# Kernel tuning notes

Measured on AMD Instinct MI355X. Metric: run time of the kernel, lower is better.

The kernel has to match this reference:

```python
import jax, jax.numpy as jnp
import numpy as np


def setup_inputs() -> dict:
    key = jax.random.key(0)
    ks = jax.random.split(key, 8)
    B, T, V, D, H, C = 1024, 80, 50000, 300, 300, 3
    sent = jax.random.randint(ks[0], (B, T), 0, V, dtype=jnp.int32)
    lens = jax.random.randint(ks[1], (B,), 1, T + 1, dtype=jnp.int32)
    emb = jax.random.normal(ks[2], (V, D), dtype=jnp.float32) * 0.1
    Wx = jax.random.normal(ks[3], (D, 4 * H), dtype=jnp.float32) * 0.05
    Wh = jax.random.normal(ks[4], (H, 4 * H), dtype=jnp.float32) * 0.05
    b = jnp.zeros((4 * H,), dtype=jnp.float32)
    Wout = jax.random.normal(ks[5], (H, C), dtype=jnp.float32) * 0.05
    bout = jnp.zeros((C,), dtype=jnp.float32)
    return {"sent": sent, "lens": lens, "emb": emb, "Wx": Wx, "Wh": Wh,
            "b": b, "Wout": Wout, "bout": bout}


def _lstm_masked(x, mask, Wx, Wh, b, H):
    # x: [B, T, D], mask: [B, T] float. Scan over time keeping h,c in carry.
    B = x.shape[0]
    h0 = jnp.zeros((B, H), dtype=x.dtype)
    c0 = jnp.zeros((B, H), dtype=x.dtype)

    def step(carry, inp):
        h, c = carry
        xt, mt = inp                      # xt: [B, D], mt: [B]
        gates = xt @ Wx + h @ Wh + b      # [B, 4H]
        i, f, g, o = jnp.split(gates, 4, axis=-1)
        i, f, o = jax.nn.sigmoid(i), jax.nn.sigmoid(f), jax.nn.sigmoid(o)
        g = jnp.tanh(g)
        c_new = f * c + i * g
        h_new = o * jnp.tanh(c_new)
        m = mt[:, None]
        h = m * h_new + (1.0 - m) * h     # mask-based state blending
        c = m * c_new + (1.0 - m) * c
        return (h, c), None

    xs = (jnp.swapaxes(x, 0, 1), jnp.swapaxes(mask, 0, 1))  # time-major
    (h, c), _ = jax.lax.scan(step, (h0, c0), xs)
    return h


def reference(sent, lens, emb, Wx, Wh, b, Wout, bout):
    T = sent.shape[1]
    H = Wh.shape[0]
    x = emb[sent]                                         # [B, T, D]
    mask = (jnp.arange(T)[None, :] < lens[:, None]).astype(x.dtype)  # [B, T]
    h = _lstm_masked(x, mask, Wx, Wh, b, H)
    logit = h @ Wout + bout                               # [B, C]
    return logit
```

## Files before the change

### kernel.cpp

```cpp
#include <hip/hip_runtime.h>
#include <hip/hip_fp16.h>


typedef float    f32x4 __attribute__((ext_vector_type(4)));
typedef _Float16 f16;
typedef _Float16 f16x8 __attribute__((ext_vector_type(8)));
typedef unsigned long long u64;
typedef unsigned int       u32;

#define NB    1024
#define TT    80
#define NV    50000
#define ND    300
#define KP    320
#define NKT   10
#define SL    75
#define SLP   80
#define NTPG  5
#define NTIL  20
#define TPB   256
#define GRID  256
#define NSLAB 8

#define TAGMASK 0x0001000100010001ULL

#define OFF_EMB   0
#define OFF_WHP   32000000
#define OFF_WXP   32819200
#define OFF_HBUF  33638400
#define HBUF_SZ   (NB * KP)
#define OFF_HF32  38881280
#define WS_NEED   40110080

__global__ __launch_bounds__(256) void absa_prep_emb(
    const float* __restrict__ emb, f16* __restrict__ embb) {
  int i = blockIdx.x * 256 + threadIdx.x;
  if (i >= NV * KP / 8) return;
  int flat = i * 8;
  int row  = flat / KP;
  int k    = flat - row * KP;
  f16x8 o;
  if (k + 7 < ND) {
    float4 a = *reinterpret_cast<const float4*>(emb + row * ND + k);
    float4 b = *reinterpret_cast<const float4*>(emb + row * ND + k + 4);
    o[0] = (f16)a.x; o[1] = (f16)a.y; o[2] = (f16)a.z; o[3] = (f16)a.w;
    o[4] = (f16)b.x; o[5] = (f16)b.y; o[6] = (f16)b.z; o[7] = (f16)b.w;
  } else {
#pragma unroll
    for (int e = 0; e < 8; ++e) {
      int kk = k + e;
      float v = (kk < ND) ? emb[row * ND + kk] : (kk == ND ? 1.0f : 0.0f);
      o[e] = (f16)v;
    }
  }
  *reinterpret_cast<f16x8*>(embb + flat) = o;
}

__global__ __launch_bounds__(256) void absa_prep_pack2(
    const float* __restrict__ Wx, const float* __restrict__ Wh,
    const float* __restrict__ bias,
    f16* __restrict__ wxp, f16* __restrict__ whp) {
  const int half = 4 * NTIL * NKT * 512;
  int idx0 = blockIdx.x * 256 + threadIdx.x;
  if (idx0 >= 2 * half) return;
  int mode = idx0 >= half;
  int idx  = idx0 - mode * half;
  int e    = idx & 7;
  int lane = (idx >> 3) & 63;
  int fid  = idx >> 9;
  int kt   = fid % NKT;
  int rem  = fid / NKT;
  int nt   = rem % NTIL;
  int n    = rem / NTIL;
  int gi   = nt / NTPG, ti = nt - gi * NTPG;
  int k    = kt * 32 + (lane >> 4) * 8 + e;
  int cc   = ti * 16 + (lane & 15);
  float v = 0.f;
  if (cc < SL) {
    int col = gi * 300 + n * SL + cc;
    if (mode == 0) {
      if (k < ND)       v = Wx[k * 1200 + col];
      else if (k == ND) v = bias[col];
    } else {
      int kl = k % SLP, n2 = k / SLP;
      if (kl < SL)      v = Wh[(n2 * SL + kl) * 1200 + col];
    }
  }
  (mode ? whp : wxp)[idx] = (f16)v;
}

__device__ __forceinline__ float sigf(float x) {
  return __builtin_amdgcn_rcpf(1.f + __builtin_amdgcn_exp2f(-1.44269504f * x));
}
__device__ __forceinline__ float tanhf_(float x) {
  float xx = fminf(15.f, fmaxf(-15.f, x));
  return 1.f - 2.f * __builtin_amdgcn_rcpf(1.f + __builtin_amdgcn_exp2f(2.88539008f * xx));
}

__device__ __forceinline__ u64 tag_pat(int tg) {
  return ((u64)(tg & 1)) | ((u64)((tg >> 1) & 1) << 16) |
         ((u64)((tg >> 2) & 1) << 32) | ((u64)((tg >> 3) & 1) << 48);
}

__global__ __launch_bounds__(TPB, 1) void absa_lstm(
    const int* __restrict__ sent, const int* __restrict__ lens,
    const f16* __restrict__ embb,
    const f16* __restrict__ whp, const f16* __restrict__ wxp,
    f16* __restrict__ hbuf, float* __restrict__ hf32) {
  const int bid = blockIdx.x;
  const int s   = bid & 7;
  const int q   = bid >> 3;
  const int n   = q & 3;
  const int g   = s * 8 + (q >> 2);

  const int tid = threadIdx.x;
  const int w   = tid >> 6;
  const int l   = tid & 63;
  const int l15 = l & 15, lk = l >> 4;
  const int grow0 = g * 16;

  __shared__ float gates[2 * 4 * 80 * 20];
  __shared__ float c_lds[80 * 20];
  __shared__ float hf_lds[80 * 20];
  __shared__ int   sent_lds[16 * TT];
  __shared__ int   len_lds[16];

  for (int i = tid; i < 16 * TT; i += TPB) sent_lds[i] = sent[g * 16 * TT + i];
  if (tid < 16) len_lds[tid] = lens[grow0 + tid];
  for (int i = tid; i < 80 * 20; i += TPB) { c_lds[i] = 0.f; hf_lds[i] = 0.f; }
  __syncthreads();

  int maxlen = 0;
#pragma unroll
  for (int r = 0; r < 16; ++r) maxlen = max(maxlen, len_lds[r]);

  f16x8 wh[NTPG][NKT];
#pragma unroll
  for (int j = 0; j < NTPG; ++j)
#pragma unroll
    for (int kt = 0; kt < NKT; ++kt)
      wh[j][kt] = *reinterpret_cast<const f16x8*>(
          whp + ((size_t)(n * NTIL + (w * NTPG + j)) * NKT + kt) * 512 + l * 8);

  int gaddr[NTPG];
#pragma unroll
  for (int j = 0; j < NTPG; ++j)
    gaddr[j] = ((w * 80) + j * 16 + l15) * 20 + lk * 4;

  f32x4 acc[NTPG];

  auto xpart = [&](int t) {
#pragma unroll
    for (int j = 0; j < NTPG; ++j) acc[j] = (f32x4){0.f, 0.f, 0.f, 0.f};
    f16x8 xa[NKT];
    const int srow = sent_lds[l15 * TT + t];
#pragma unroll
    for (int kt = 0; kt < NKT; ++kt)
      xa[kt] = *reinterpret_cast<const f16x8*>(embb + (size_t)srow * KP + kt * 32 + lk * 8);
#pragma unroll
    for (int j = 0; j < NTPG; ++j) {
      f16x8 wxa[NKT];
#pragma unroll
      for (int kt = 0; kt < NKT; ++kt)
        wxa[kt] = *reinterpret_cast<const f16x8*>(
            wxp + ((size_t)(n * NTIL + (w * NTPG + j)) * NKT + kt) * 512 + l * 8);
#pragma unroll
      for (int kt = 0; kt < NKT; ++kt)
        acc[j] = __builtin_amdgcn_mfma_f32_16x16x32_f16(xa[kt], wxa[kt], acc[j], 0, 0, 0);
    }
  };

  xpart(0);

  for (int t = 0; t < maxlen; ++t) {
    const int par = (t & 1) * (4 * 80 * 20);

    if (t > 0) {
      const u64 expv = tag_pat((t - 1) % 15);
      const f16* hp = hbuf + (size_t)((t - 1) & 7) * HBUF_SZ + (grow0 + l15) * KP + lk * 8;
      u64 q0[NKT], q1[NKT];
#pragma unroll
      for (int kt = 0; kt < NKT; ++kt) {
        const u64* p = reinterpret_cast<const u64*>(hp + kt * 32);
        q0[kt] = __hip_atomic_load(p,     __ATOMIC_RELAXED, __HIP_MEMORY_SCOPE_AGENT);
        q1[kt] = __hip_atomic_load(p + 1, __ATOMIC_RELAXED, __HIP_MEMORY_SCOPE_AGENT);
      }
#pragma unroll
      for (int kt = 0; kt < NKT; ++kt) {
        const u64* p = reinterpret_cast<const u64*>(hp + kt * 32);
        int sp = 0;
        while ((q0[kt] & TAGMASK) != expv && ++sp < (1 << 18))
          q0[kt] = __hip_atomic_load(p,     __ATOMIC_RELAXED, __HIP_MEMORY_SCOPE_AGENT);
        sp = 0;
        while ((q1[kt] & TAGMASK) != expv && ++sp < (1 << 18))
          q1[kt] = __hip_atomic_load(p + 1, __ATOMIC_RELAXED, __HIP_MEMORY_SCOPE_AGENT);
        union { u64 qq[2]; f16x8 v; } u;
        u.qq[0] = q0[kt]; u.qq[1] = q1[kt];
#pragma unroll
        for (int j = 0; j < NTPG; ++j)
          acc[j] = __builtin_amdgcn_mfma_f32_16x16x32_f16(u.v, wh[j][kt], acc[j], 0, 0, 0);
      }
    }

#pragma unroll
    for (int j = 0; j < NTPG; ++j)
      *reinterpret_cast<f32x4*>(&gates[par + gaddr[j]]) = acc[j];
    __syncthreads();

    {
      const u64 pat = tag_pat(t % 15);
      f16* hc = hbuf + (size_t)(t & 7) * HBUF_SZ;
      for (int i = tid; i < 320; i += TPB) {
        int row = i & 15, qd = i >> 4;
        union { unsigned short us[4]; u64 uu; } pu;
#pragma unroll
        for (int e = 0; e < 4; ++e) {
          int cc = qd * 4 + e;
          float h = 0.f;
          if (cc < SL) {
            int base = cc * 20 + row;
            if (t < len_lds[row]) {
              float vi = gates[par + (0 * 80 + cc) * 20 + row];
              float vf = gates[par + (1 * 80 + cc) * 20 + row];
              float vg = gates[par + (2 * 80 + cc) * 20 + row];
              float vo = gates[par + (3 * 80 + cc) * 20 + row];
              float iv = sigf(vi), fv = sigf(vf), ov = sigf(vo);
              float gv = tanhf_(vg);
              float cn = fv * c_lds[base] + iv * gv;
              h = ov * tanhf_(cn);
              c_lds[base] = cn;
              hf_lds[base] = h;
            } else {
              h = hf_lds[base];
            }
          }
          union { f16 f; unsigned short u; } cv;
          cv.f = (f16)h;
          pu.us[e] = cv.u;
        }
        pu.uu = (pu.uu & ~TAGMASK) | pat;
        u64* dst = reinterpret_cast<u64*>(hc + (size_t)(grow0 + row) * KP + n * SLP + qd * 4);
        __hip_atomic_store(dst, pu.uu, __ATOMIC_RELAXED, __HIP_MEMORY_SCOPE_AGENT);
      }
    }

    if (t + 1 < maxlen) xpart(t + 1);
  }

  __syncthreads();
  for (int i = tid; i < 16 * SL; i += TPB) {
    int row = i & 15, cc = i >> 4;
    hf32[(grow0 + row) * ND + n * SL + cc] = hf_lds[cc * 20 + row];
  }
}

__global__ __launch_bounds__(256) void absa_logits(
    const float* __restrict__ hf32, const float* __restrict__ Wout,
    const float* __restrict__ bout, float* __restrict__ out) {
  int row = blockIdx.x * 4 + (threadIdx.x >> 6);
  int l   = threadIdx.x & 63;
  float s0 = 0.f, s1 = 0.f, s2 = 0.f;
  for (int k = l; k < ND; k += 64) {
    float h  = hf32[row * ND + k];
    s0 += h * Wout[k * 3 + 0];
    s1 += h * Wout[k * 3 + 1];
    s2 += h * Wout[k * 3 + 2];
  }
#pragma unroll
  for (int o = 32; o; o >>= 1) {
    s0 += __shfl_down(s0, o);
    s1 += __shfl_down(s1, o);
    s2 += __shfl_down(s2, o);
  }
  if (l == 0) {
    out[row * 3 + 0] = s0 + bout[0];
    out[row * 3 + 1] = s1 + bout[1];
    out[row * 3 + 2] = s2 + bout[2];
  }
}

extern "C" void kernel_launch(void* const* d_in, const int* in_sizes, int n_in,
                              void* d_out, int out_size, void* d_ws, size_t ws_size,
                              hipStream_t stream) {
  const int*   sent = (const int*)d_in[0];
  const int*   lens = (const int*)d_in[1];
  const float* emb  = (const float*)d_in[2];
  const float* Wx   = (const float*)d_in[3];
  const float* Wh   = (const float*)d_in[4];
  const float* bv   = (const float*)d_in[5];
  const float* Wout = (const float*)d_in[6];
  const float* bout = (const float*)d_in[7];
  float* out = (float*)d_out;

  char* wsb = (char*)d_ws;
  f16*   embb = (f16*)(wsb + OFF_EMB);
  f16*   whp  = (f16*)(wsb + OFF_WHP);
  f16*   wxp  = (f16*)(wsb + OFF_WXP);
  f16*   hbuf = (f16*)(wsb + OFF_HBUF);
  float* hf32 = (float*)(wsb + OFF_HF32);

  (void)hipMemsetAsync(hbuf, 0xFF, NSLAB * NB * KP * 2, stream);

  absa_prep_emb  <<<(NV * KP / 8 + 255) / 256, 256, 0, stream>>>(emb, embb);
  absa_prep_pack2<<<2 * 4 * NTIL * NKT * 512 / 256, 256, 0, stream>>>(Wx, Wh, bv, wxp, whp);
  absa_lstm      <<<GRID, TPB, 0, stream>>>(sent, lens, embb, whp, wxp, hbuf, hf32);
  absa_logits    <<<NB / 4, 256, 0, stream>>>(hf32, Wout, bout, out);
}
```

Before: 758.6 us.

## Keep Wx in registers, prefetch next h tile before xpart, batch tag polling

Wx fragments are loaded into registers once, next to Wh, instead of being reloaded from global memory every time step, and the x-part loop is reordered so each embedding fragment feeds all tiles. The next step's h loads are issued before the x-part MFMAs so their latency overlaps that compute. The per-element spin loops become a single loop that re-polls only the fragments whose tags are still stale. This doubles the register footprint for weights (100 f16x8 vectors), which risks spills or lower occupancy, and prefetched values that turn out stale still need re-polling.

```diff
diff --git a/kernel.cpp b/kernel.cpp
--- a/kernel.cpp
+++ b/kernel.cpp
@@ -6,7 +6,6 @@
 typedef _Float16 f16;
 typedef _Float16 f16x8 __attribute__((ext_vector_type(8)));
 typedef unsigned long long u64;
-typedef unsigned int       u32;
 
 #define NB    1024
 #define TT    80
@@ -134,13 +133,15 @@
 #pragma unroll
   for (int r = 0; r < 16; ++r) maxlen = max(maxlen, len_lds[r]);
 
-  f16x8 wh[NTPG][NKT];
+  f16x8 wh[NTPG][NKT], wx[NTPG][NKT];
 #pragma unroll
   for (int j = 0; j < NTPG; ++j)
 #pragma unroll
-    for (int kt = 0; kt < NKT; ++kt)
-      wh[j][kt] = *reinterpret_cast<const f16x8*>(
-          whp + ((size_t)(n * NTIL + (w * NTPG + j)) * NKT + kt) * 512 + l * 8);
+    for (int kt = 0; kt < NKT; ++kt) {
+      size_t off = ((size_t)(n * NTIL + (w * NTPG + j)) * NKT + kt) * 512 + l * 8;
+      wh[j][kt] = *reinterpret_cast<const f16x8*>(whp + off);
+      wx[j][kt] = *reinterpret_cast<const f16x8*>(wxp + off);
+    }
 
   int gaddr[NTPG];
 #pragma unroll
@@ -148,25 +149,19 @@
     gaddr[j] = ((w * 80) + j * 16 + l15) * 20 + lk * 4;
 
   f32x4 acc[NTPG];
+  u64 q0[NKT], q1[NKT];
 
   auto xpart = [&](int t) {
 #pragma unroll
     for (int j = 0; j < NTPG; ++j) acc[j] = (f32x4){0.f, 0.f, 0.f, 0.f};
-    f16x8 xa[NKT];
     const int srow = sent_lds[l15 * TT + t];
-#pragma unroll
-    for (int kt = 0; kt < NKT; ++kt)
-      xa[kt] = *reinterpret_cast<const f16x8*>(embb + (size_t)srow * KP + kt * 32 + lk * 8);
-#pragma unroll
-    for (int j = 0; j < NTPG; ++j) {
-      f16x8 wxa[NKT];
-#pragma unroll
-      for (int kt = 0; kt < NKT; ++kt)
-        wxa[kt] = *reinterpret_cast<const f16x8*>(
-            wxp + ((size_t)(n * NTIL + (w * NTPG + j)) * NKT + kt) * 512 + l * 8);
-#pragma unroll
-      for (int kt = 0; kt < NKT; ++kt)
-        acc[j] = __builtin_amdgcn_mfma_f32_16x16x32_f16(xa[kt], wxa[kt], acc[j], 0, 0, 0);
+    const f16* xb = embb + (size_t)srow * KP + lk * 8;
+#pragma unroll
+    for (int kt = 0; kt < NKT; ++kt) {
+      f16x8 xa = *reinterpret_cast<const f16x8*>(xb + kt * 32);
+#pragma unroll
+      for (int j = 0; j < NTPG; ++j)
+        acc[j] = __builtin_amdgcn_mfma_f32_16x16x32_f16(xa, wx[j][kt], acc[j], 0, 0, 0);
     }
   };
 
@@ -178,22 +173,25 @@
     if (t > 0) {
       const u64 expv = tag_pat((t - 1) % 15);
       const f16* hp = hbuf + (size_t)((t - 1) & 7) * HBUF_SZ + (grow0 + l15) * KP + lk * 8;
-      u64 q0[NKT], q1[NKT];
+      bool any = true;
+      int guard = 0;
+      while (any && guard++ < (1 << 14)) {
+        any = false;
+#pragma unroll
+        for (int kt = 0; kt < NKT; ++kt) {
+          const u64* p = reinterpret_cast<const u64*>(hp + kt * 32);
+          if ((q0[kt] & TAGMASK) != expv) {
+            q0[kt] = __hip_atomic_load(p,     __ATOMIC_RELAXED, __HIP_MEMORY_SCOPE_AGENT);
+            any = true;
+          }
+          if ((q1[kt] & TAGMASK) != expv) {
+            q1[kt] = __hip_atomic_load(p + 1, __ATOMIC_RELAXED, __HIP_MEMORY_SCOPE_AGENT);
+            any = true;
+          }
+        }
+      }
 #pragma unroll
       for (int kt = 0; kt < NKT; ++kt) {
-        const u64* p = reinterpret_cast<const u64*>(hp + kt * 32);
-        q0[kt] = __hip_atomic_load(p,     __ATOMIC_RELAXED, __HIP_MEMORY_SCOPE_AGENT);
-        q1[kt] = __hip_atomic_load(p + 1, __ATOMIC_RELAXED, __HIP_MEMORY_SCOPE_AGENT);
-      }
-#pragma unroll
-      for (int kt = 0; kt < NKT; ++kt) {
-        const u64* p = reinterpret_cast<const u64*>(hp + kt * 32);
-        int sp = 0;
-        while ((q0[kt] & TAGMASK) != expv && ++sp < (1 << 18))
-          q0[kt] = __hip_atomic_load(p,     __ATOMIC_RELAXED, __HIP_MEMORY_SCOPE_AGENT);
-        sp = 0;
-        while ((q1[kt] & TAGMASK) != expv && ++sp < (1 << 18))
-          q1[kt] = __hip_atomic_load(p + 1, __ATOMIC_RELAXED, __HIP_MEMORY_SCOPE_AGENT);
         union { u64 qq[2]; f16x8 v; } u;
         u.qq[0] = q0[kt]; u.qq[1] = q1[kt];
 #pragma unroll
@@ -244,7 +242,17 @@
       }
     }
 
-    if (t + 1 < maxlen) xpart(t + 1);
+    if (t + 1 < maxlen) {
+      const f16* hpn = hbuf + (size_t)(t & 7) * HBUF_SZ + (grow0 + l15) * KP + lk * 8;
+#pragma unroll
+      for (int kt = 0; kt < NKT; ++kt) {
+        const u64* p = reinterpret_cast<const u64*>(hpn + kt * 32);
+        q0[kt] = __hip_atomic_load(p,     __ATOMIC_RELAXED, __HIP_MEMORY_SCOPE_AGENT);
+        q1[kt] = __hip_atomic_load(p + 1, __ATOMIC_RELAXED, __HIP_MEMORY_SCOPE_AGENT);
+      }
+      __builtin_amdgcn_sched_barrier(0);
+      xpart(t + 1);
+    }
   }
 
   __syncthreads();
```

Result: slower. 1.041 ms (+37.2%).
